# Performance work log

Measured on AMD Instinct MI355X. Metric: run time of the kernel, lower is better.

## Reference

```python
import jax, jax.numpy as jnp
import numpy as np

N_NODES = 100000
N_EDGES = 1600000
IN_CH = 1024
FEAT_CH = 128
OUT_CH = 3


def setup_inputs() -> dict:
    key = jax.random.key(0)
    ks = jax.random.split(key, 9)
    features = jax.random.normal(ks[0], (N_NODES, IN_CH), dtype=jnp.float32)
    edges = jax.random.randint(ks[1], (2, N_EDGES), 0, N_NODES, dtype=jnp.int64)
    edges2 = jax.random.randint(ks[2], (2, N_EDGES), 0, N_NODES, dtype=jnp.int64)
    edge_features = jax.random.normal(ks[3], (N_EDGES, 1), dtype=jnp.float32)
    additional_feature = jax.random.normal(ks[4], (N_NODES, 20), dtype=jnp.float32)
    # GCNConv linear weights (glorot-ish scale) and biases
    W1 = jax.random.normal(ks[5], (IN_CH, FEAT_CH), dtype=jnp.float32) * (1.0 / np.sqrt(IN_CH))
    b1 = jnp.zeros((FEAT_CH,), dtype=jnp.float32)
    W2 = jax.random.normal(ks[6], (FEAT_CH, OUT_CH), dtype=jnp.float32) * (1.0 / np.sqrt(FEAT_CH))
    b2 = jnp.zeros((OUT_CH,), dtype=jnp.float32)
    return {"features": features, "edges": edges, "edges2": edges2,
            "edge_features": edge_features, "additional_feature": additional_feature,
            "W1": W1, "b1": b1, "W2": W2, "b2": b2}


def gcn_conv(x, edge_index, W, b, num_nodes):
    """PyG GCNConv: x' = D^{-1/2}(A+I)D^{-1/2} x W + b (self-loops added)."""
    x = x @ W  # project first (cheaper feature dim for aggregation)
    loop = jnp.arange(num_nodes, dtype=edge_index.dtype)
    src = jnp.concatenate([edge_index[0], loop])
    dst = jnp.concatenate([edge_index[1], loop])
    deg = jax.ops.segment_sum(jnp.ones_like(dst, dtype=x.dtype), dst,
                              num_segments=num_nodes)  # >=1 due to self-loops
    dinv = jax.lax.rsqrt(deg)
    norm = dinv[src] * dinv[dst]  # [E+N]
    out = jax.ops.segment_sum(x[src] * norm[:, None], dst, num_segments=num_nodes)
    return out + b


def reference(features, edges, edges2, edge_features, additional_feature, W1, b1, W2, b2):
    # use_additional_channels=False -> features unchanged; edge_features forced to None
    n = features.shape[0]
    x = gcn_conv(features, edges2, W1, b1, n)
    x = jax.nn.relu(x)
    # dropout inactive in eval mode
    return gcn_conv(x, edges2, W2, b2, n)
```

## Files before the change

### kernel.cpp

```cpp
#include <hip/hip_runtime.h>
#include <hip/hip_bf16.h>

typedef __attribute__((ext_vector_type(8))) _Float16 half8;
typedef __attribute__((ext_vector_type(4))) float f32x4;

#define N_NODES 100000
#define N_EDGES 1600000
#define IN_CH 1024
#define FEAT 128
#define CAP 64
#define NDIG 196
#define CAPC 10240
#define NTILES ((N_NODES + 127) / 128)

__global__ void k_prep(const float* __restrict__ W1, _Float16* __restrict__ W1t,
                       int* __restrict__ cursorC, int* __restrict__ done) {
    int idx = blockIdx.x * 256 + threadIdx.x;
    if (idx < IN_CH * FEAT) {
        int col = idx & (FEAT - 1);
        int k = idx >> 7;
        W1t[(size_t)col * IN_CH + k] = (_Float16)W1[idx];
    }
    if (idx < NDIG) cursorC[idx] = idx * CAPC;
    if (idx == 0) *done = 0;
}

__global__ __launch_bounds__(256, 2) void k_build_gemm(
    const float* __restrict__ A, const _Float16* __restrict__ Bt,
    const int4* __restrict__ src4, const int4* __restrict__ dst4,
    int* __restrict__ cursorC, uint2* __restrict__ recs,
    int* __restrict__ csr, int* __restrict__ cnt, int* __restrict__ done,
    _Float16* __restrict__ H, int M, int e4)
{
    __shared__ union {
        _Float16 Bs[2][128][72];
        struct { int hist[NDIG], segoff[NDIG], lcur[NDIG]; } bin;
        int cl[512];
    } sm;
    const int t = threadIdx.x;

    if (blockIdx.x < NDIG) {
        const int b = blockIdx.x;
        if (t < NDIG) sm.bin.hist[t] = 0;
        __syncthreads();

        const int base4 = b * 2048;
        int4 sv[8], dv[8];
#pragma unroll
        for (int j = 0; j < 8; ++j) {
            int idx = base4 + j * 256 + t;
            if (idx < e4) { sv[j] = src4[idx]; dv[j] = dst4[idx]; }
            else { sv[j] = (int4){-1,-1,-1,-1}; dv[j] = (int4){-1,-1,-1,-1}; }
        }
#pragma unroll
        for (int j = 0; j < 8; ++j) {
            int dd[4] = {dv[j].x, dv[j].y, dv[j].z, dv[j].w};
            int ss[4] = {sv[j].x, sv[j].y, sv[j].z, sv[j].w};
#pragma unroll
            for (int c = 0; c < 4; ++c)
                if ((unsigned)dd[c] < N_NODES && (unsigned)ss[c] < N_NODES)
                    atomicAdd(&sm.bin.hist[dd[c] >> 9], 1);
        }
        __syncthreads();
        if (t < NDIG) {
            sm.bin.segoff[t] = atomicAdd(&cursorC[t], sm.bin.hist[t]);
            sm.bin.lcur[t] = 0;
        }
        __syncthreads();
#pragma unroll
        for (int j = 0; j < 8; ++j) {
            int dd[4] = {dv[j].x, dv[j].y, dv[j].z, dv[j].w};
            int ss[4] = {sv[j].x, sv[j].y, sv[j].z, sv[j].w};
#pragma unroll
            for (int c = 0; c < 4; ++c) {
                if ((unsigned)dd[c] < N_NODES && (unsigned)ss[c] < N_NODES) {
                    int dg = dd[c] >> 9;
                    int r = atomicAdd(&sm.bin.lcur[dg], 1);
                    int pos = sm.bin.segoff[dg] + r;
                    if (pos < (dg + 1) * CAPC)
                        recs[pos] = (uint2){(unsigned)ss[c], (unsigned)dd[c]};
                }
            }
        }
        __syncthreads();
        if (t == 0) {
            __threadfence();
            __hip_atomic_fetch_add(done, 1, __ATOMIC_RELEASE, __HIP_MEMORY_SCOPE_AGENT);
            while (__hip_atomic_load(done, __ATOMIC_ACQUIRE, __HIP_MEMORY_SCOPE_AGENT) < NDIG)
                __builtin_amdgcn_s_sleep(8);
        }
        __syncthreads();
        const int d = blockIdx.x;
        for (int j = t; j < 512; j += 256) sm.cl[j] = 0;
        __syncthreads();
        const int base = d * CAPC;
        int n = cursorC[d] - base;
        if (n > CAPC) n = CAPC;
        for (int k = t; k < n; k += 256) {
            uint2 r = recs[base + k];
            int local = (int)r.y & 511;
            int slot = atomicAdd(&sm.cl[local], 1);
            if (slot < CAP) csr[((int)r.y << 6) + slot] = (int)r.x;
        }
        __syncthreads();
        const int node0 = d << 9;
        for (int j = t; j < 512; j += 256) {
            int node = node0 + j;
            if (node < N_NODES) cnt[node] = sm.cl[j] < CAP ? sm.cl[j] : CAP;
        }
        return;
    }

    const int wid = t >> 6, lane = t & 63;
    const int brow0 = (blockIdx.x - NDIG) * 128;
    const int NKT = IN_CH / 64;

    f32x4 acc[2][8];
#pragma unroll
    for (int m = 0; m < 2; ++m)
#pragma unroll
        for (int nn = 0; nn < 8; ++nn) acc[m][nn] = (f32x4){0.f, 0.f, 0.f, 0.f};

    int r0 = brow0 + wid * 32 + (lane & 15);
    int r1 = r0 + 16;
    if (r0 >= M) r0 = M - 1;
    if (r1 >= M) r1 = M - 1;
    const int kbase = (lane >> 4) * 8;
    const float* pa0 = A + (size_t)r0 * IN_CH + kbase;
    const float* pa1 = A + (size_t)r1 * IN_CH + kbase;
    const int bcol = t >> 1;
    const int bko = (t & 1) * 32;
    const _Float16* pb = Bt + (size_t)bcol * IN_CH + bko;

    float4 ar[2][2][2];
    half8 af[2][2];
    half8 bst[4];

#define LOAD_A(kt)                                                              \
    {                                                                           \
        _Pragma("unroll") for (int m = 0; m < 2; ++m) {                         \
            const float* p_ = (m ? pa1 : pa0) + (kt) * 64;                      \
            _Pragma("unroll") for (int kk = 0; kk < 2; ++kk) {                  \
                ar[m][kk][0] = *(const float4*)(p_ + kk * 32);                  \
                ar[m][kk][1] = *(const float4*)(p_ + kk * 32 + 4);              \
            }                                                                   \
        }                                                                       \
    }
#define CVT_A()                                                                 \
    {                                                                           \
        _Pragma("unroll") for (int m = 0; m < 2; ++m)                           \
        _Pragma("unroll") for (int kk = 0; kk < 2; ++kk) {                      \
            half8 h;                                                            \
            h[0] = (_Float16)ar[m][kk][0].x; h[1] = (_Float16)ar[m][kk][0].y;   \
            h[2] = (_Float16)ar[m][kk][0].z; h[3] = (_Float16)ar[m][kk][0].w;   \
            h[4] = (_Float16)ar[m][kk][1].x; h[5] = (_Float16)ar[m][kk][1].y;   \
            h[6] = (_Float16)ar[m][kk][1].z; h[7] = (_Float16)ar[m][kk][1].w;   \
            af[m][kk] = h;                                                      \
        }                                                                       \
    }
#define LOAD_B(kt)                                                              \
    {                                                                           \
        const half8* s_ = (const half8*)(pb + (kt) * 64);                       \
        _Pragma("unroll") for (int j = 0; j < 4; ++j) bst[j] = s_[j];           \
    }
#define WRITE_B(buf)                                                            \
    {                                                                           \
        _Pragma("unroll") for (int j = 0; j < 4; ++j)                           \
            *(half8*)(&sm.Bs[buf][bcol][bko + j * 8]) = bst[j];                 \
    }

    LOAD_A(0); LOAD_B(0);
    CVT_A();
    WRITE_B(0);
    __syncthreads();

    for (int kt = 0; kt < NKT; ++kt) {
        const int cur = kt & 1;
        const bool more = (kt + 1 < NKT);
        if (more) { LOAD_B(kt + 1); LOAD_A(kt + 1); }
#pragma unroll
        for (int kk = 0; kk < 2; ++kk) {
            half8 a0 = af[0][kk], a1 = af[1][kk];
#pragma unroll
            for (int nn = 0; nn < 8; ++nn) {
                half8 bb = *(const half8*)(&sm.Bs[cur][nn * 16 + (lane & 15)][kk * 32 + kbase]);
                acc[0][nn] = __builtin_amdgcn_mfma_f32_16x16x32_f16(a0, bb, acc[0][nn], 0, 0, 0);
                acc[1][nn] = __builtin_amdgcn_mfma_f32_16x16x32_f16(a1, bb, acc[1][nn], 0, 0, 0);
            }
        }
        if (more) {
            CVT_A();
            WRITE_B(cur ^ 1);
            __syncthreads();
        }
    }
#undef LOAD_A
#undef CVT_A
#undef LOAD_B
#undef WRITE_B

    int colb = lane & 15, rgrp = (lane >> 4) * 4;
#pragma unroll
    for (int m = 0; m < 2; ++m) {
#pragma unroll
        for (int r = 0; r < 4; ++r) {
            int grow = brow0 + wid * 32 + m * 16 + rgrp + r;
            if (grow < M) {
                _Float16* hp = H + (size_t)grow * FEAT + colb;
#pragma unroll
                for (int nn = 0; nn < 8; ++nn) hp[nn * 16] = (_Float16)acc[m][nn][r];
            }
        }
    }
}

__device__ __forceinline__ float dinv_of(const int* cnt, int i, int& m) {
    m = cnt[i];
    return rsqrtf((float)(m + 1));
}

__global__ __launch_bounds__(256) void k_agg1(const _Float16* __restrict__ H,
                                              const int* __restrict__ csr,
                                              const int* __restrict__ cnt,
                                              const float* __restrict__ b1,
                                              const float* __restrict__ W2,
                                              float* __restrict__ Y, int n) {
    int wid = threadIdx.x >> 6, lane = threadIdx.x & 63;
    int i = blockIdx.x * 4 + wid;
    if (i >= n) return;
    const int g = lane >> 4, u = lane & 15;
    int m;
    float di = dinv_of(cnt, i, m);
    int base = i << 6;

    int sl; float dl;
    if (lane < m) {
        sl = csr[base + lane];
        int cs = cnt[sl];
        dl = rsqrtf((float)(cs + 1));
    } else {
        sl = i;
        dl = (lane == m) ? di : 0.f;
    }
    int mm = (m < 63 ? m : 63) + 1;

    float ax[8];
#pragma unroll
    for (int j = 0; j < 8; ++j) ax[j] = 0.f;

    for (int e = 0; e < mm; e += 8) {
        int i0 = e + g, i1 = e + 4 + g;
        bool v0 = i0 < mm, v1 = i1 < mm;
        int c0i = v0 ? i0 : 0, c1i = v1 ? i1 : 0;
        int s0 = __shfl(sl, c0i);
        float w0 = __shfl(dl, c0i);
        int s1 = __shfl(sl, c1i);
        float w1 = __shfl(dl, c1i);
        if (!v0) { s0 = i; w0 = 0.f; }
        if (!v1) { s1 = i; w1 = 0.f; }
        half8 h0 = *(const half8*)(H + ((size_t)s0 << 7) + u * 8);
        half8 h1 = *(const half8*)(H + ((size_t)s1 << 7) + u * 8);
#pragma unroll
        for (int j = 0; j < 8; ++j) ax[j] += w0 * (float)h0[j] + w1 * (float)h1[j];
    }

#pragma unroll
    for (int j = 0; j < 8; ++j) {
        ax[j] += __shfl_xor(ax[j], 16);
        ax[j] += __shfl_xor(ax[j], 32);
    }

    int c0 = u * 8;
    float y0 = 0.f, y1 = 0.f, y2 = 0.f;
#pragma unroll
    for (int j = 0; j < 8; ++j) {
        float x = di * ax[j] + b1[c0 + j];
        x = x > 0.f ? x : 0.f;
        y0 += x * W2[(c0 + j) * 3 + 0];
        y1 += x * W2[(c0 + j) * 3 + 1];
        y2 += x * W2[(c0 + j) * 3 + 2];
    }
#pragma unroll
    for (int d = 1; d < 16; d <<= 1) {
        y0 += __shfl_xor(y0, d);
        y1 += __shfl_xor(y1, d);
        y2 += __shfl_xor(y2, d);
    }
    if (lane == 0) {
        float* yp = Y + (size_t)i * 4;
        yp[0] = di * y0; yp[1] = di * y1; yp[2] = di * y2;
    }
}

__global__ void k_agg2(const float* __restrict__ Y, const int* __restrict__ csr,
                       const int* __restrict__ cnt, const float* __restrict__ b2,
                       float* __restrict__ out, int n) {
    int i = blockIdx.x * 256 + threadIdx.x;
    if (i >= n) return;
    int m;
    float di = dinv_of(cnt, i, m);
    int base = i << 6;
    const float4* Y4 = (const float4*)Y;
    float4 self = Y4[i];
    float a0 = self.x, a1 = self.y, a2 = self.z;
    int e = 0;
    for (; e + 1 < m; e += 2) {
        int s0 = csr[base + e], s1 = csr[base + e + 1];
        float4 v0 = Y4[s0], v1 = Y4[s1];
        a0 += v0.x + v1.x;
        a1 += v0.y + v1.y;
        a2 += v0.z + v1.z;
    }
    if (e < m) {
        float4 v0 = Y4[csr[base + e]];
        a0 += v0.x; a1 += v0.y; a2 += v0.z;
    }
    out[(size_t)i * 3 + 0] = di * a0 + b2[0];
    out[(size_t)i * 3 + 1] = di * a1 + b2[1];
    out[(size_t)i * 3 + 2] = di * a2 + b2[2];
}

extern "C" void kernel_launch(void* const* d_in, const int* in_sizes, int n_in,
                              void* d_out, int out_size, void* d_ws, size_t ws_size,
                              hipStream_t stream) {
    const float* features = (const float*)d_in[0];
    const int* edges2 = (const int*)d_in[2];
    const float* W1 = (const float*)d_in[5];
    const float* b1 = (const float*)d_in[6];
    const float* W2 = (const float*)d_in[7];
    const float* b2 = (const float*)d_in[8];
    float* out = (float*)d_out;

    const int N = N_NODES, E = N_EDGES;
    const int* srcp = edges2;
    const int* dstp = edges2 + E;

    char* p = (char*)d_ws;
    auto carve = [&](size_t bytes) { char* q = p; p += (bytes + 255) & ~(size_t)255; return q; };
    int* cnt      = (int*)carve(4 * (size_t)N);
    int* cursorC  = (int*)carve(4 * NDIG);
    int* done     = (int*)carve(4);
    uint2* recs   = (uint2*)carve(8 * (size_t)NDIG * CAPC);
    int* csr      = (int*)carve(4 * (size_t)N * CAP);
    _Float16* W1t = (_Float16*)carve(2 * (size_t)IN_CH * FEAT);
    _Float16* H   = (_Float16*)carve(2 * (size_t)N * FEAT);
    float* Y      = (float*)carve(16 * (size_t)N);

    k_prep<<<dim3(512), dim3(256), 0, stream>>>(W1, W1t, cursorC, done);
    k_build_gemm<<<dim3(NDIG + NTILES), dim3(256), 0, stream>>>(
        features, W1t, (const int4*)srcp, (const int4*)dstp,
        cursorC, recs, csr, cnt, done, H, N, E / 4);
    k_agg1<<<dim3((N + 3) / 4), dim3(256), 0, stream>>>(H, csr, cnt, b1, W2, Y, N);
    k_agg2<<<dim3((N + 255) / 256), dim3(256), 0, stream>>>(Y, csr, cnt, b2, out, N);
}
```

Measured before the change: 269.5 us.

## Precompute dinv array, widen gather unroll in aggregations, raise GEMM occupancy bound

The build kernel now writes a per-node dinv array next to the degree counts, so the aggregation kernels load it directly instead of recomputing rsqrt from cnt for each neighbour. k_agg1 now gathers four H rows per iteration instead of two, and k_agg2 processes four neighbours per iteration. This gives more memory-level parallelism in both gathers. Raising launch_bounds for the fused build/GEMM kernel from 2 to 3 waves per SIMD limits registers and may cause spills in the GEMM tiles.

```diff
diff --git a/kernel.cpp b/kernel.cpp
--- a/kernel.cpp
+++ b/kernel.cpp
@@ -17,20 +17,19 @@
                        int* __restrict__ cursorC, int* __restrict__ done) {
     int idx = blockIdx.x * 256 + threadIdx.x;
     if (idx < IN_CH * FEAT) {
-        int col = idx & (FEAT - 1);
-        int k = idx >> 7;
+        int col = idx & (FEAT - 1), k = idx >> 7;
         W1t[(size_t)col * IN_CH + k] = (_Float16)W1[idx];
     }
     if (idx < NDIG) cursorC[idx] = idx * CAPC;
     if (idx == 0) *done = 0;
 }
 
-__global__ __launch_bounds__(256, 2) void k_build_gemm(
+__global__ __launch_bounds__(256, 3) void k_build_gemm(
     const float* __restrict__ A, const _Float16* __restrict__ Bt,
     const int4* __restrict__ src4, const int4* __restrict__ dst4,
     int* __restrict__ cursorC, uint2* __restrict__ recs,
-    int* __restrict__ csr, int* __restrict__ cnt, int* __restrict__ done,
-    _Float16* __restrict__ H, int M, int e4)
+    int* __restrict__ csr, int* __restrict__ cnt, float* __restrict__ dinvarr,
+    int* __restrict__ done, _Float16* __restrict__ H, int M, int e4)
 {
     __shared__ union {
         _Float16 Bs[2][128][72];
@@ -43,7 +42,6 @@
         const int b = blockIdx.x;
         if (t < NDIG) sm.bin.hist[t] = 0;
         __syncthreads();
-
         const int base4 = b * 2048;
         int4 sv[8], dv[8];
 #pragma unroll
@@ -106,7 +104,11 @@
         const int node0 = d << 9;
         for (int j = t; j < 512; j += 256) {
             int node = node0 + j;
-            if (node < N_NODES) cnt[node] = sm.cl[j] < CAP ? sm.cl[j] : CAP;
+            if (node < N_NODES) {
+                int c = sm.cl[j] < CAP ? sm.cl[j] : CAP;
+                cnt[node] = c;
+                dinvarr[node] = rsqrtf((float)(c + 1));
+            }
         }
         return;
     }
@@ -214,14 +216,10 @@
     }
 }
 
-__device__ __forceinline__ float dinv_of(const int* cnt, int i, int& m) {
-    m = cnt[i];
-    return rsqrtf((float)(m + 1));
-}
-
 __global__ __launch_bounds__(256) void k_agg1(const _Float16* __restrict__ H,
                                               const int* __restrict__ csr,
                                               const int* __restrict__ cnt,
+                                              const float* __restrict__ dinvarr,
                                               const float* __restrict__ b1,
                                               const float* __restrict__ W2,
                                               float* __restrict__ Y, int n) {
@@ -229,39 +227,39 @@
     int i = blockIdx.x * 4 + wid;
     if (i >= n) return;
     const int g = lane >> 4, u = lane & 15;
-    int m;
-    float di = dinv_of(cnt, i, m);
-    int base = i << 6;
+    int m = cnt[i];
+    float di = dinvarr[i];
 
     int sl; float dl;
-    if (lane < m) {
-        sl = csr[base + lane];
-        int cs = cnt[sl];
-        dl = rsqrtf((float)(cs + 1));
-    } else {
-        sl = i;
-        dl = (lane == m) ? di : 0.f;
-    }
+    if (lane < m) { sl = csr[(i << 6) + lane]; dl = dinvarr[sl]; }
+    else          { sl = i;                    dl = (lane == m) ? di : 0.f; }
     int mm = (m < 63 ? m : 63) + 1;
 
     float ax[8];
 #pragma unroll
     for (int j = 0; j < 8; ++j) ax[j] = 0.f;
 
-    for (int e = 0; e < mm; e += 8) {
-        int i0 = e + g, i1 = e + 4 + g;
-        bool v0 = i0 < mm, v1 = i1 < mm;
-        int c0i = v0 ? i0 : 0, c1i = v1 ? i1 : 0;
-        int s0 = __shfl(sl, c0i);
-        float w0 = __shfl(dl, c0i);
-        int s1 = __shfl(sl, c1i);
-        float w1 = __shfl(dl, c1i);
+    for (int e = 0; e < mm; e += 16) {
+        int idx0 = e + g, idx1 = e + 4 + g, idx2 = e + 8 + g, idx3 = e + 12 + g;
+        bool v0 = idx0 < mm, v1 = idx1 < mm, v2 = idx2 < mm, v3 = idx3 < mm;
+        int c0i = v0 ? idx0 : 0, c1i = v1 ? idx1 : 0;
+        int c2i = v2 ? idx2 : 0, c3i = v3 ? idx3 : 0;
+        int s0 = __shfl(sl, c0i); float w0 = __shfl(dl, c0i);
+        int s1 = __shfl(sl, c1i); float w1 = __shfl(dl, c1i);
+        int s2 = __shfl(sl, c2i); float w2 = __shfl(dl, c2i);
+        int s3 = __shfl(sl, c3i); float w3 = __shfl(dl, c3i);
         if (!v0) { s0 = i; w0 = 0.f; }
         if (!v1) { s1 = i; w1 = 0.f; }
+        if (!v2) { s2 = i; w2 = 0.f; }
+        if (!v3) { s3 = i; w3 = 0.f; }
         half8 h0 = *(const half8*)(H + ((size_t)s0 << 7) + u * 8);
         half8 h1 = *(const half8*)(H + ((size_t)s1 << 7) + u * 8);
-#pragma unroll
-        for (int j = 0; j < 8; ++j) ax[j] += w0 * (float)h0[j] + w1 * (float)h1[j];
+        half8 h2 = *(const half8*)(H + ((size_t)s2 << 7) + u * 8);
+        half8 h3 = *(const half8*)(H + ((size_t)s3 << 7) + u * 8);
+#pragma unroll
+        for (int j = 0; j < 8; ++j)
+            ax[j] += w0 * (float)h0[j] + w1 * (float)h1[j]
+                   + w2 * (float)h2[j] + w3 * (float)h3[j];
     }
 
 #pragma unroll
@@ -293,25 +291,26 @@
 }
 
 __global__ void k_agg2(const float* __restrict__ Y, const int* __restrict__ csr,
-                       const int* __restrict__ cnt, const float* __restrict__ b2,
-                       float* __restrict__ out, int n) {
+                       const int* __restrict__ cnt, const float* __restrict__ dinvarr,
+                       const float* __restrict__ b2, float* __restrict__ out, int n) {
     int i = blockIdx.x * 256 + threadIdx.x;
     if (i >= n) return;
-    int m;
-    float di = dinv_of(cnt, i, m);
+    int m = cnt[i];
+    float di = dinvarr[i];
     int base = i << 6;
     const float4* Y4 = (const float4*)Y;
     float4 self = Y4[i];
     float a0 = self.x, a1 = self.y, a2 = self.z;
     int e = 0;
-    for (; e + 1 < m; e += 2) {
-        int s0 = csr[base + e], s1 = csr[base + e + 1];
-        float4 v0 = Y4[s0], v1 = Y4[s1];
-        a0 += v0.x + v1.x;
-        a1 += v0.y + v1.y;
-        a2 += v0.z + v1.z;
-    }
-    if (e < m) {
+    for (; e + 3 < m; e += 4) {
+        int s0 = csr[base + e],     s1 = csr[base + e + 1];
+        int s2 = csr[base + e + 2], s3 = csr[base + e + 3];
+        float4 v0 = Y4[s0], v1 = Y4[s1], v2 = Y4[s2], v3 = Y4[s3];
+        a0 += (v0.x + v1.x) + (v2.x + v3.x);
+        a1 += (v0.y + v1.y) + (v2.y + v3.y);
+        a2 += (v0.z + v1.z) + (v2.z + v3.z);
+    }
+    for (; e < m; ++e) {
         float4 v0 = Y4[csr[base + e]];
         a0 += v0.x; a1 += v0.y; a2 += v0.z;
     }
@@ -332,24 +331,25 @@
     float* out = (float*)d_out;
 
     const int N = N_NODES, E = N_EDGES;
-    const int* srcp = edges2;
-    const int* dstp = edges2 + E;
+    const int4* src4 = (const int4*)edges2;
+    const int4* dst4 = (const int4*)(edges2 + E);
+    int e4 = E / 4;
 
     char* p = (char*)d_ws;
     auto carve = [&](size_t bytes) { char* q = p; p += (bytes + 255) & ~(size_t)255; return q; };
-    int* cnt      = (int*)carve(4 * (size_t)N);
-    int* cursorC  = (int*)carve(4 * NDIG);
-    int* done     = (int*)carve(4);
-    uint2* recs   = (uint2*)carve(8 * (size_t)NDIG * CAPC);
-    int* csr      = (int*)carve(4 * (size_t)N * CAP);
-    _Float16* W1t = (_Float16*)carve(2 * (size_t)IN_CH * FEAT);
-    _Float16* H   = (_Float16*)carve(2 * (size_t)N * FEAT);
-    float* Y      = (float*)carve(16 * (size_t)N);
+    int* cnt       = (int*)carve(4 * (size_t)N);
+    float* dinvarr = (float*)carve(4 * (size_t)N);
+    int* cursorC   = (int*)carve(4 * NDIG);
+    int* done      = (int*)carve(4);
+    uint2* recs    = (uint2*)carve(8 * (size_t)NDIG * CAPC);
+    int* csr       = (int*)carve(4 * (size_t)N * CAP);
+    _Float16* W1t  = (_Float16*)carve(2 * (size_t)IN_CH * FEAT);
+    _Float16* H    = (_Float16*)carve(2 * (size_t)N * FEAT);
+    float* Y       = (float*)carve(16 * (size_t)N);
 
     k_prep<<<dim3(512), dim3(256), 0, stream>>>(W1, W1t, cursorC, done);
     k_build_gemm<<<dim3(NDIG + NTILES), dim3(256), 0, stream>>>(
-        features, W1t, (const int4*)srcp, (const int4*)dstp,
-        cursorC, recs, csr, cnt, done, H, N, E / 4);
-    k_agg1<<<dim3((N + 3) / 4), dim3(256), 0, stream>>>(H, csr, cnt, b1, W2, Y, N);
-    k_agg2<<<dim3((N + 255) / 256), dim3(256), 0, stream>>>(Y, csr, cnt, b2, out, N);
-}
+        features, W1t, src4, dst4, cursorC, recs, csr, cnt, dinvarr, done, H, N, e4);
+    k_agg1<<<dim3((N + 3) / 4), dim3(256), 0, stream>>>(H, csr, cnt, dinvarr, b1, W2, Y, N);
+    k_agg2<<<dim3((N + 255) / 256), dim3(256), 0, stream>>>(Y, csr, cnt, dinvarr, b2, out, N);
+}
```

Result: no change. 273.4 us (+1.5%).
